# Kernel optimization log

Measured on AMD Instinct MI355X. Metric: run time of the kernel, lower is better.

## Reference

```python
import jax, jax.numpy as jnp
import numpy as np

B, T, C = 2, 2048, 1024
NH, NKV, HD = 16, 4, 64   # n_head, n_kv_head, head_dim
WIN_LEFT = 1024           # flash-attn window_size=(1024, 0), causal


def rmsnorm(x):
    # F.rms_norm with no weight: x / sqrt(mean(x^2) + eps), eps = dtype eps
    eps = jnp.finfo(x.dtype).eps
    return x * jax.lax.rsqrt(jnp.mean(x * x, axis=-1, keepdims=True) + eps)


def rope(x, cos, sin):
    # x: [B,T,H,D]; cos/sin: [T,1,D/2] broadcast over batch and heads
    d = x.shape[-1] // 2
    x1, x2 = x[..., :d], x[..., d:]
    return jnp.concatenate([x1 * cos + x2 * sin, -x1 * sin + x2 * cos], axis=-1)


def setup_inputs() -> dict:
    key = jax.random.key(0)
    ks = jax.random.split(key, 9)
    return {
        "x":  jax.random.normal(ks[0], (B, T, C), jnp.float32),
        "x0": jax.random.normal(ks[1], (B, T, C), jnp.float32),
        "ve": jax.random.normal(ks[2], (B, T, NKV, HD), jnp.float32),
        "cos": jax.random.normal(ks[3], (T, 1, HD // 2), jnp.float32),
        "sin": jax.random.normal(ks[4], (T, 1, HD // 2), jnp.float32),
        "Wq": jax.random.normal(ks[5], (NH * HD, C), jnp.float32) * 0.02,
        "Wk": jax.random.normal(ks[6], (NKV * HD, C), jnp.float32) * 0.02,
        "Wv": jax.random.normal(ks[7], (NKV * HD, C), jnp.float32) * 0.02,
        "Wo": jax.random.normal(ks[8], (C, C), jnp.float32) * 0.02,
    }


def reference(x, x0, ve, cos, sin, Wq, Wk, Wv, Wo):
    b, t, c = x.shape
    q = (x @ Wq.T).reshape(b, t, NH, HD)
    k = (x @ Wk.T).reshape(b, t, NKV, HD)
    v = (x @ Wv.T).reshape(b, t, NKV, HD)
    v_init = v
    # is_late branch: halve_value, add_init_qkv, add_init_v all active
    v = 0.5 * v
    x0n = rmsnorm(x0)
    q = 0.5 * q + 0.5 * (x0n @ Wq.T).reshape(b, t, NH, HD)
    k = 0.5 * k + 0.5 * (x0n @ Wk.T).reshape(b, t, NKV, HD)
    v = v + 0.5 * (x0n @ Wv.T).reshape(b, t, NKV, HD)
    v = v + 0.5 * ve
    # rotary -> rms-norm -> scale 1.2 on q and k
    q = rmsnorm(rope(q, cos, sin)) * 1.2
    k = rmsnorm(rope(k, cos, sin)) * 1.2
    # GQA: repeat kv heads to match query heads
    g = NH // NKV
    k = jnp.repeat(k, g, axis=2)
    v = jnp.repeat(v, g, axis=2)
    scores = jnp.einsum("bqhd,bkhd->bhqk", q, k) / np.float32(np.sqrt(HD))
    i = jnp.arange(t)[:, None]
    j = jnp.arange(t)[None, :]
    mask = (j <= i) & (i - j <= WIN_LEFT)  # causal sliding window
    scores = jnp.where(mask, scores, jnp.finfo(scores.dtype).min)
    att = jax.nn.softmax(scores, axis=-1)
    y = jnp.einsum("bhqk,bkhd->bqhd", att, v).reshape(b, t, c)
    y = y @ Wo.T
    return (y, v_init)
```

## Files before the change

kernel.cpp:

```cpp
#include <hip/hip_runtime.h>


typedef __attribute__((ext_vector_type(8))) short bf16x8;
typedef __attribute__((ext_vector_type(4))) float f32x4;
typedef unsigned short u16;
typedef unsigned int u32;

#define B_ 2
#define T_ 2048
#define C_ 1024
#define NH_ 16
#define NKV_ 4
#define HD_ 64
#define WIN_ 1024
#define M_ (B_*T_)
#define EPS_ 1.1920929e-07f

__device__ __forceinline__ u16 f2bf(float f) {
  u32 u = __float_as_uint(f);
  u32 r = (u + 0x7fffu + ((u >> 16) & 1u)) >> 16;
  return (u16)r;
}
__device__ __forceinline__ float bf2f(u16 h) { return __uint_as_float(((u32)h) << 16); }

__global__ __launch_bounds__(256) void k_convert(const float* __restrict__ src,
                                                 u16* __restrict__ dst, int n4) {
  int i = blockIdx.x * 256 + threadIdx.x;
  if (i >= n4) return;
  float4 v = ((const float4*)src)[i];
  ushort4 o;
  o.x = f2bf(v.x); o.y = f2bf(v.y); o.z = f2bf(v.z); o.w = f2bf(v.w);
  ((ushort4*)dst)[i] = o;
}

__global__ __launch_bounds__(256) void k_rms_combine(const float* __restrict__ x,
                                                     const float* __restrict__ x0,
                                                     u16* __restrict__ xbf,
                                                     u16* __restrict__ xmbf) {
  int row = blockIdx.x;
  int tid = threadIdx.x, lane = tid & 63, w = tid >> 6;
  const float4* px0 = (const float4*)(x0 + (size_t)row * C_);
  const float4* px  = (const float4*)(x  + (size_t)row * C_);
  float4 v0 = px0[tid];
  float ss = v0.x * v0.x + v0.y * v0.y + v0.z * v0.z + v0.w * v0.w;
  #pragma unroll
  for (int m = 1; m < 64; m <<= 1) ss += __shfl_xor(ss, m, 64);
  __shared__ float red[4];
  if (lane == 0) red[w] = ss;
  __syncthreads();
  float tot = red[0] + red[1] + red[2] + red[3];
  float rn = rsqrtf(tot * (1.0f / C_) + EPS_);
  float4 vx = px[tid];
  ushort4 om, ox;
  om.x = f2bf(0.5f * (vx.x + v0.x * rn));
  om.y = f2bf(0.5f * (vx.y + v0.y * rn));
  om.z = f2bf(0.5f * (vx.z + v0.z * rn));
  om.w = f2bf(0.5f * (vx.w + v0.w * rn));
  ox.x = f2bf(vx.x); ox.y = f2bf(vx.y); ox.z = f2bf(vx.z); ox.w = f2bf(vx.w);
  ((ushort4*)(xmbf + (size_t)row * C_))[tid] = om;
  ((ushort4*)(xbf  + (size_t)row * C_))[tid] = ox;
}

__device__ __forceinline__ void gemm_core(const u16* __restrict__ pa,
                                          const u16* __restrict__ pw,
                                          u16 (*As)[40], u16 (*Ws)[40],
                                          int lane, int r0, int c0,
                                          int ra, int ka, int rw, int kw,
                                          f32x4 acc[4][2]) {
  for (int kt = 0; kt < 1024; kt += 32) {
    int4 a0 = *(const int4*)(pa + kt);
    int4 a1 = *(const int4*)(pa + kt + 8);
    int4 w0 = *(const int4*)(pw + kt);
    __syncthreads();
    *(int4*)&As[ra][ka]     = a0;
    *(int4*)&As[ra][ka + 8] = a1;
    *(int4*)&Ws[rw][kw]     = w0;
    __syncthreads();
    bf16x8 af[4], bfr[2];
    #pragma unroll
    for (int fi = 0; fi < 4; fi++)
      af[fi] = *(const bf16x8*)&As[r0 + fi * 16 + (lane & 15)][(lane >> 4) * 8];
    #pragma unroll
    for (int fj = 0; fj < 2; fj++)
      bfr[fj] = *(const bf16x8*)&Ws[c0 + fj * 16 + (lane & 15)][(lane >> 4) * 8];
    #pragma unroll
    for (int fi = 0; fi < 4; fi++)
      #pragma unroll
      for (int fj = 0; fj < 2; fj++)
        acc[fi][fj] = __builtin_amdgcn_mfma_f32_16x16x32_bf16(af[fi], bfr[fj], acc[fi][fj], 0, 0, 0);
  }
}

__global__ __launch_bounds__(256) void k_gemm_qkv(const u16* __restrict__ xm,
                                                  const u16* __restrict__ xb,
                                                  const u16* __restrict__ Wq,
                                                  const u16* __restrict__ Wk,
                                                  const u16* __restrict__ Wv,
                                                  u16* __restrict__ qpre,
                                                  u16* __restrict__ kpre,
                                                  u16* __restrict__ vmid,
                                                  float* __restrict__ vinit) {
  __shared__ u16 As[128][40];
  __shared__ u16 Ws[64][40];
  int tid = threadIdx.x, lane = tid & 63, w = tid >> 6;
  int m0 = blockIdx.x * 128, bn = blockIdx.y, n0 = bn * 64;
  const u16* A; const u16* Wseg; int nseg;
  if (bn < 16)      { A = xm; Wseg = Wq; nseg = n0; }
  else if (bn < 20) { A = xm; Wseg = Wk; nseg = n0 - 1024; }
  else if (bn < 24) { A = xm; Wseg = Wv; nseg = n0 - 1280; }
  else              { A = xb; Wseg = Wv; nseg = n0 - 1536; }
  int ra = tid >> 1, ka = (tid & 1) * 16;
  int rw = tid >> 2, kw = (tid & 3) * 8;
  const u16* pa = A + (size_t)(m0 + ra) * 1024 + ka;
  const u16* pw = Wseg + (size_t)(nseg + rw) * 1024 + kw;
  int r0 = (w >> 1) * 64, c0 = (w & 1) * 32;
  f32x4 acc[4][2] = {};
  gemm_core(pa, pw, As, Ws, lane, r0, c0, ra, ka, rw, kw, acc);
  #pragma unroll
  for (int fi = 0; fi < 4; fi++)
    #pragma unroll
    for (int fj = 0; fj < 2; fj++)
      #pragma unroll
      for (int i = 0; i < 4; i++) {
        int m = m0 + r0 + fi * 16 + (lane >> 4) * 4 + i;
        int nl = nseg + c0 + fj * 16 + (lane & 15);
        float v = acc[fi][fj][i];
        if (bn < 16)      qpre[(size_t)m * 1024 + nl] = f2bf(v);
        else if (bn < 20) kpre[(size_t)m * 256 + nl] = f2bf(v);
        else if (bn < 24) vmid[(size_t)m * 256 + nl] = f2bf(v);
        else              vinit[(size_t)m * 256 + nl] = v;
      }
}

__global__ __launch_bounds__(256) void k_gemm_o(const u16* __restrict__ A,
                                                const u16* __restrict__ W,
                                                float* __restrict__ y) {
  __shared__ u16 As[128][40];
  __shared__ u16 Ws[64][40];
  int tid = threadIdx.x, lane = tid & 63, w = tid >> 6;
  int m0 = blockIdx.x * 128, n0 = blockIdx.y * 64;
  int ra = tid >> 1, ka = (tid & 1) * 16;
  int rw = tid >> 2, kw = (tid & 3) * 8;
  const u16* pa = A + (size_t)(m0 + ra) * 1024 + ka;
  const u16* pw = W + (size_t)(n0 + rw) * 1024 + kw;
  int r0 = (w >> 1) * 64, c0 = (w & 1) * 32;
  f32x4 acc[4][2] = {};
  gemm_core(pa, pw, As, Ws, lane, r0, c0, ra, ka, rw, kw, acc);
  #pragma unroll
  for (int fi = 0; fi < 4; fi++)
    #pragma unroll
    for (int fj = 0; fj < 2; fj++)
      #pragma unroll
      for (int i = 0; i < 4; i++) {
        int m = m0 + r0 + fi * 16 + (lane >> 4) * 4 + i;
        int n = n0 + c0 + fj * 16 + (lane & 15);
        y[(size_t)m * 1024 + n] = acc[fi][fj][i];
      }
}

__global__ __launch_bounds__(256) void k_qkv_post(const u16* __restrict__ qpre,
                                                  const u16* __restrict__ kpre,
                                                  const u16* __restrict__ vmid,
                                                  const float* __restrict__ ve,
                                                  const float* __restrict__ cosp,
                                                  const float* __restrict__ sinp,
                                                  u16* __restrict__ Qh,
                                                  u16* __restrict__ Kh,
                                                  u16* __restrict__ Vh) {
  int w = threadIdx.x >> 6, lane = threadIdx.x & 63;
  int vid = blockIdx.x * 4 + w;
  const int NQ = B_ * T_ * NH_;
  const int NK = B_ * T_ * NKV_;
  if (vid < NQ + NK) {
    int t, dstoff;
    float val;
    if (vid < NQ) {
      int h = vid & 15; t = (vid >> 4) & 2047; int b = vid >> 15;
      val = bf2f(qpre[(size_t)vid * 64 + lane]);
      dstoff = 0;
      size_t dst = (((size_t)(b * NH_ + h) * T_) + t) * 64 + lane;
      int di = lane & 31;
      float partner = __shfl_xor(val, 32, 64);
      float c = cosp[t * 32 + di], s = sinp[t * 32 + di];
      float r = (lane < 32) ? (val * c + partner * s) : (val * c - partner * s);
      float ss = r * r;
      #pragma unroll
      for (int m2 = 1; m2 < 64; m2 <<= 1) ss += __shfl_xor(ss, m2, 64);
      r *= rsqrtf(ss * (1.0f / 64.0f) + EPS_) * 1.2f;
      Qh[dst] = f2bf(r);
      (void)dstoff;
      return;
    } else {
      int kid = vid - NQ;
      int hk = kid & 3; t = (kid >> 2) & 2047; int b = kid >> 13;
      val = bf2f(kpre[(size_t)kid * 64 + lane]);
      size_t dst = (((size_t)(b * NKV_ + hk) * T_) + t) * 64 + lane;
      int di = lane & 31;
      float partner = __shfl_xor(val, 32, 64);
      float c = cosp[t * 32 + di], s = sinp[t * 32 + di];
      float r = (lane < 32) ? (val * c + partner * s) : (val * c - partner * s);
      float ss = r * r;
      #pragma unroll
      for (int m2 = 1; m2 < 64; m2 <<= 1) ss += __shfl_xor(ss, m2, 64);
      r *= rsqrtf(ss * (1.0f / 64.0f) + EPS_) * 1.2f;
      Kh[dst] = f2bf(r);
      return;
    }
  } else {
    int vvid = vid - NQ - NK;
    int hk = vvid & 3; int t = (vvid >> 2) & 2047; int b = vvid >> 13;
    float v = bf2f(vmid[(size_t)vvid * 64 + lane]) + 0.5f * ve[(size_t)vvid * 64 + lane];
    Vh[(((size_t)(b * NKV_ + hk) * T_) + t) * 64 + lane] = f2bf(v);
  }
}

__global__ __launch_bounds__(256) void k_attn(const u16* __restrict__ Qh,
                                              const u16* __restrict__ Kh,
                                              const u16* __restrict__ Vh,
                                              u16* __restrict__ ao) {
  __shared__ u16 Ks[64][72];
  __shared__ u16 Vt[64][72];
  __shared__ u16 Ps[4][16][72];
  int tid = threadIdx.x, lane = tid & 63, w = tid >> 6;
  int qt = blockIdx.x, h = blockIdx.y, b = blockIdx.z;
  int hk = h >> 2;
  const u16* Qp = Qh + ((size_t)(b * NH_ + h) * T_) * 64;
  const u16* Kp = Kh + ((size_t)(b * NKV_ + hk) * T_) * 64;
  const u16* Vp = Vh + ((size_t)(b * NKV_ + hk) * T_) * 64;
  int q0 = qt * 64;
  int qr = q0 + w * 16 + (lane & 15);
  bf16x8 qf[2];
  qf[0] = *(const bf16x8*)(Qp + (size_t)qr * 64 + (lane >> 4) * 8);
  qf[1] = *(const bf16x8*)(Qp + (size_t)qr * 64 + 32 + (lane >> 4) * 8);
  f32x4 o[4] = {};
  float mrun[4], lrun[4];
  #pragma unroll
  for (int i = 0; i < 4; i++) { mrun[i] = -1e4f; lrun[i] = 0.f; }
  int kt_lo = q0 - WIN_; if (kt_lo < 0) kt_lo = 0;
  int rk = tid >> 2, dk = (tid & 3) * 16;
  int kp2 = tid >> 3, dv = (tid & 7) * 8;
  for (int kt = kt_lo; kt <= q0; kt += 64) {
    int4 kv0 = *(const int4*)(Kp + (size_t)(kt + rk) * 64 + dk);
    int4 kv1 = *(const int4*)(Kp + (size_t)(kt + rk) * 64 + dk + 8);
    int4 va  = *(const int4*)(Vp + (size_t)(kt + 2 * kp2) * 64 + dv);
    int4 vb  = *(const int4*)(Vp + (size_t)(kt + 2 * kp2 + 1) * 64 + dv);
    __syncthreads();
    *(int4*)&Ks[rk][dk]     = kv0;
    *(int4*)&Ks[rk][dk + 8] = kv1;
    {
      const u16* sa = (const u16*)&va;
      const u16* sb = (const u16*)&vb;
      #pragma unroll
      for (int j = 0; j < 8; j++) {
        u32 valp = (u32)sa[j] | ((u32)sb[j] << 16);
        *(u32*)&Vt[dv + j][2 * kp2] = valp;
      }
    }
    __syncthreads();
    f32x4 s[4];
    #pragma unroll
    for (int ct = 0; ct < 4; ct++) {
      f32x4 z = {0.f, 0.f, 0.f, 0.f};
      s[ct] = z;
      #pragma unroll
      for (int kk = 0; kk < 2; kk++) {
        bf16x8 kf = *(const bf16x8*)&Ks[ct * 16 + (lane & 15)][kk * 32 + (lane >> 4) * 8];
        s[ct] = __builtin_amdgcn_mfma_f32_16x16x32_bf16(qf[kk], kf, s[ct], 0, 0, 0);
      }
    }
    int irow_base = q0 + w * 16 + (lane >> 4) * 4;
    float tmax[4];
    #pragma unroll
    for (int i = 0; i < 4; i++) tmax[i] = -1e30f;
    #pragma unroll
    for (int ct = 0; ct < 4; ct++) {
      int j = kt + ct * 16 + (lane & 15);
      #pragma unroll
      for (int i = 0; i < 4; i++) {
        int irow = irow_base + i;
        bool valid = (j <= irow) && (irow - j <= WIN_);
        float sv = valid ? s[ct][i] * 0.125f : -1e9f;
        s[ct][i] = sv;
        tmax[i] = fmaxf(tmax[i], sv);
      }
    }
    #pragma unroll
    for (int i = 0; i < 4; i++) {
      #pragma unroll
      for (int m2 = 1; m2 < 16; m2 <<= 1) tmax[i] = fmaxf(tmax[i], __shfl_xor(tmax[i], m2, 64));
    }
    float alpha[4];
    #pragma unroll
    for (int i = 0; i < 4; i++) {
      float mn = fmaxf(mrun[i], tmax[i]);
      alpha[i] = __expf(mrun[i] - mn);
      mrun[i] = mn;
    }
    float rsum[4] = {0.f, 0.f, 0.f, 0.f};
    #pragma unroll
    for (int ct = 0; ct < 4; ct++)
      #pragma unroll
      for (int i = 0; i < 4; i++) {
        float p = __expf(s[ct][i] - mrun[i]);
        s[ct][i] = p;
        rsum[i] += p;
      }
    #pragma unroll
    for (int i = 0; i < 4; i++) {
      #pragma unroll
      for (int m2 = 1; m2 < 16; m2 <<= 1) rsum[i] += __shfl_xor(rsum[i], m2, 64);
      lrun[i] = lrun[i] * alpha[i] + rsum[i];
    }
    #pragma unroll
    for (int fj = 0; fj < 4; fj++)
      #pragma unroll
      for (int i = 0; i < 4; i++) o[fj][i] *= alpha[i];
    #pragma unroll
    for (int ct = 0; ct < 4; ct++)
      #pragma unroll
      for (int i = 0; i < 4; i++)
        Ps[w][(lane >> 4) * 4 + i][ct * 16 + (lane & 15)] = f2bf(s[ct][i]);
    bf16x8 pf[2];
    pf[0] = *(const bf16x8*)&Ps[w][lane & 15][(lane >> 4) * 8];
    pf[1] = *(const bf16x8*)&Ps[w][lane & 15][32 + (lane >> 4) * 8];
    #pragma unroll
    for (int fj = 0; fj < 4; fj++) {
      #pragma unroll
      for (int ks = 0; ks < 2; ks++) {
        bf16x8 vf = *(const bf16x8*)&Vt[fj * 16 + (lane & 15)][ks * 32 + (lane >> 4) * 8];
        o[fj] = __builtin_amdgcn_mfma_f32_16x16x32_bf16(pf[ks], vf, o[fj], 0, 0, 0);
      }
    }
  }
  #pragma unroll
  for (int i = 0; i < 4; i++) {
    float inv = 1.0f / lrun[i];
    int irow = q0 + w * 16 + (lane >> 4) * 4 + i;
    size_t base = ((size_t)(b * T_ + irow) * NH_ + h) * 64;
    #pragma unroll
    for (int fj = 0; fj < 4; fj++)
      ao[base + fj * 16 + (lane & 15)] = f2bf(o[fj][i] * inv);
  }
}

extern "C" void kernel_launch(void* const* d_in, const int* in_sizes, int n_in,
                              void* d_out, int out_size, void* d_ws, size_t ws_size,
                              hipStream_t stream) {
  const float* x    = (const float*)d_in[0];
  const float* x0   = (const float*)d_in[1];
  const float* ve   = (const float*)d_in[2];
  const float* cosp = (const float*)d_in[3];
  const float* sinp = (const float*)d_in[4];
  const float* Wq   = (const float*)d_in[5];
  const float* Wk   = (const float*)d_in[6];
  const float* Wv   = (const float*)d_in[7];
  const float* Wo   = (const float*)d_in[8];
  float* out = (float*)d_out;

  u16* ws = (u16*)d_ws;
  size_t off = 0;
  u16* xbf  = ws + off; off += (size_t)M_ * C_;
  u16* xmbf = ws + off; off += (size_t)M_ * C_;
  u16* Wqb  = ws + off; off += (size_t)1024 * 1024;
  u16* Wkb  = ws + off; off += (size_t)256 * 1024;
  u16* Wvb  = ws + off; off += (size_t)256 * 1024;
  u16* Wob  = ws + off; off += (size_t)1024 * 1024;
  u16* qpre = ws + off; off += (size_t)M_ * 1024;
  u16* kpre = ws + off; off += (size_t)M_ * 256;
  u16* vmid = ws + off; off += (size_t)M_ * 256;
  u16* Vhb  = ws + off; off += (size_t)B_ * NKV_ * T_ * 64;
  u16* aob = xbf;
  u16* Qhb = xmbf;
  u16* Khb = Wqb;

  k_convert<<<1024, 256, 0, stream>>>(Wq, Wqb, 1024 * 1024 / 4);
  k_convert<<<256,  256, 0, stream>>>(Wk, Wkb, 256 * 1024 / 4);
  k_convert<<<256,  256, 0, stream>>>(Wv, Wvb, 256 * 1024 / 4);
  k_convert<<<1024, 256, 0, stream>>>(Wo, Wob, 1024 * 1024 / 4);
  k_rms_combine<<<4096, 256, 0, stream>>>(x, x0, xbf, xmbf);
  k_gemm_qkv<<<dim3(32, 28), 256, 0, stream>>>(xmbf, xbf, Wqb, Wkb, Wvb,
                                               qpre, kpre, vmid, out + (size_t)M_ * C_);
  k_qkv_post<<<24576, 256, 0, stream>>>(qpre, kpre, vmid, ve, cosp, sinp, Qhb, Khb, Vhb);
  k_attn<<<dim3(T_ / 64, NH_, B_), 256, 0, stream>>>(Qhb, Khb, Vhb, aob);
  k_gemm_o<<<dim3(32, 16), 256, 0, stream>>>(aob, Wob, out);
}
```

Before: 250.6 us.

## Use direct global-to-LDS loads with swizzle, pre-transpose V, merge converts

GEMM and attention tiles are now loaded with global_load_lds straight into XOR-swizzled LDS buffers, and the GEMM K-step grows from 32 to 64. The in-kernel V transpose is replaced by a separate kernel that writes V already transposed. Attention now skips the mask arithmetic on interior tiles and launches longest query tiles first. The four weight conversions become one launch, and Q/K post-processing is split from V handling. These changes target register staging, LDS bank conflicts and launch overhead, at the cost of an extra kernel and more code complexity.

After: 218.7 us. 12.7% less time.

```diff
diff --git a/kernel.cpp b/kernel.cpp
--- a/kernel.cpp
+++ b/kernel.cpp
@@ -11,7 +11,6 @@
 #define C_ 1024
 #define NH_ 16
 #define NKV_ 4
-#define HD_ 64
 #define WIN_ 1024
 #define M_ (B_*T_)
 #define EPS_ 1.1920929e-07f
@@ -23,14 +22,28 @@
 }
 __device__ __forceinline__ float bf2f(u16 h) { return __uint_as_float(((u32)h) << 16); }
 
-__global__ __launch_bounds__(256) void k_convert(const float* __restrict__ src,
-                                                 u16* __restrict__ dst, int n4) {
-  int i = blockIdx.x * 256 + threadIdx.x;
-  if (i >= n4) return;
-  float4 v = ((const float4*)src)[i];
+__device__ __forceinline__ void gload16(const u16* g, u16* l) {
+  __builtin_amdgcn_global_load_lds((const __attribute__((address_space(1))) u32*)g,
+                                   (__attribute__((address_space(3))) u32*)l, 16, 0, 0);
+}
+#define SWZ(row, kg) ((((row)) << 7) + ((((kg) ^ ((row) & 7))) << 4))
+#define SWO(lane) (8 * (((lane) & 7) ^ (((lane) >> 3) & 7)))
+
+__global__ __launch_bounds__(256) void k_convert_all(const float* __restrict__ Wq,
+                                                     const float* __restrict__ Wk,
+                                                     const float* __restrict__ Wv,
+                                                     const float* __restrict__ Wo,
+                                                     u16* __restrict__ dst) {
+  int i4 = blockIdx.x * 256 + threadIdx.x;
+  const float* src; int s0;
+  if (i4 < 262144)      { src = Wq; s0 = 0; }
+  else if (i4 < 327680) { src = Wk; s0 = 262144; }
+  else if (i4 < 393216) { src = Wv; s0 = 327680; }
+  else                  { src = Wo; s0 = 393216; }
+  float4 v = ((const float4*)src)[i4 - s0];
   ushort4 o;
   o.x = f2bf(v.x); o.y = f2bf(v.y); o.z = f2bf(v.z); o.w = f2bf(v.w);
-  ((ushort4*)dst)[i] = o;
+  ((ushort4*)dst)[i4] = o;
 }
 
 __global__ __launch_bounds__(256) void k_rms_combine(const float* __restrict__ x,
@@ -61,33 +74,38 @@
   ((ushort4*)(xbf  + (size_t)row * C_))[tid] = ox;
 }
 
-__device__ __forceinline__ void gemm_core(const u16* __restrict__ pa,
-                                          const u16* __restrict__ pw,
-                                          u16 (*As)[40], u16 (*Ws)[40],
-                                          int lane, int r0, int c0,
-                                          int ra, int ka, int rw, int kw,
+__device__ __forceinline__ void gemm_core(const u16* pa0, const u16* pb0,
+                                          u16* Asl, u16* Bsl,
+                                          int lane, int w, int r0, int c0,
                                           f32x4 acc[4][2]) {
-  for (int kt = 0; kt < 1024; kt += 32) {
-    int4 a0 = *(const int4*)(pa + kt);
-    int4 a1 = *(const int4*)(pa + kt + 8);
-    int4 w0 = *(const int4*)(pw + kt);
+  const char* Ab = (const char*)Asl;
+  const char* Bb = (const char*)Bsl;
+  for (int kt = 0; kt < 1024; kt += 64) {
     __syncthreads();
-    *(int4*)&As[ra][ka]     = a0;
-    *(int4*)&As[ra][ka + 8] = a1;
-    *(int4*)&Ws[rw][kw]     = w0;
+    #pragma unroll
+    for (int c = 0; c < 4; c++)
+      gload16(pa0 + (size_t)c * 32 * 1024 + kt, Asl + (c * 32 + w * 8) * 64);
+    #pragma unroll
+    for (int c = 0; c < 2; c++)
+      gload16(pb0 + (size_t)c * 32 * 1024 + kt, Bsl + (c * 32 + w * 8) * 64);
     __syncthreads();
-    bf16x8 af[4], bfr[2];
-    #pragma unroll
-    for (int fi = 0; fi < 4; fi++)
-      af[fi] = *(const bf16x8*)&As[r0 + fi * 16 + (lane & 15)][(lane >> 4) * 8];
-    #pragma unroll
-    for (int fj = 0; fj < 2; fj++)
-      bfr[fj] = *(const bf16x8*)&Ws[c0 + fj * 16 + (lane & 15)][(lane >> 4) * 8];
-    #pragma unroll
-    for (int fi = 0; fi < 4; fi++)
+    bf16x8 af[2][4], bfr[2][2];
+    #pragma unroll
+    for (int ks = 0; ks < 2; ks++) {
+      #pragma unroll
+      for (int fi = 0; fi < 4; fi++)
+        af[ks][fi] = *(const bf16x8*)(Ab + SWZ(r0 + fi * 16 + (lane & 15), ks * 4 + (lane >> 4)));
       #pragma unroll
       for (int fj = 0; fj < 2; fj++)
-        acc[fi][fj] = __builtin_amdgcn_mfma_f32_16x16x32_bf16(af[fi], bfr[fj], acc[fi][fj], 0, 0, 0);
+        bfr[ks][fj] = *(const bf16x8*)(Bb + SWZ(c0 + fj * 16 + (lane & 15), ks * 4 + (lane >> 4)));
+    }
+    #pragma unroll
+    for (int ks = 0; ks < 2; ks++)
+      #pragma unroll
+      for (int fi = 0; fi < 4; fi++)
+        #pragma unroll
+        for (int fj = 0; fj < 2; fj++)
+          acc[fi][fj] = __builtin_amdgcn_mfma_f32_16x16x32_bf16(af[ks][fi], bfr[ks][fj], acc[fi][fj], 0, 0, 0);
   }
 }
 
@@ -100,8 +118,8 @@
                                                   u16* __restrict__ kpre,
                                                   u16* __restrict__ vmid,
                                                   float* __restrict__ vinit) {
-  __shared__ u16 As[128][40];
-  __shared__ u16 Ws[64][40];
+  __shared__ u16 Asl[128 * 64];
+  __shared__ u16 Bsl[64 * 64];
   int tid = threadIdx.x, lane = tid & 63, w = tid >> 6;
   int m0 = blockIdx.x * 128, bn = blockIdx.y, n0 = bn * 64;
   const u16* A; const u16* Wseg; int nseg;
@@ -109,13 +127,12 @@
   else if (bn < 20) { A = xm; Wseg = Wk; nseg = n0 - 1024; }
   else if (bn < 24) { A = xm; Wseg = Wv; nseg = n0 - 1280; }
   else              { A = xb; Wseg = Wv; nseg = n0 - 1536; }
-  int ra = tid >> 1, ka = (tid & 1) * 16;
-  int rw = tid >> 2, kw = (tid & 3) * 8;
-  const u16* pa = A + (size_t)(m0 + ra) * 1024 + ka;
-  const u16* pw = Wseg + (size_t)(nseg + rw) * 1024 + kw;
+  int swo = SWO(lane);
+  const u16* pa0 = A    + (size_t)(m0 + w * 8 + (lane >> 3)) * 1024 + swo;
+  const u16* pb0 = Wseg + (size_t)(nseg + w * 8 + (lane >> 3)) * 1024 + swo;
   int r0 = (w >> 1) * 64, c0 = (w & 1) * 32;
   f32x4 acc[4][2] = {};
-  gemm_core(pa, pw, As, Ws, lane, r0, c0, ra, ka, rw, kw, acc);
+  gemm_core(pa0, pb0, Asl, Bsl, lane, w, r0, c0, acc);
   #pragma unroll
   for (int fi = 0; fi < 4; fi++)
     #pragma unroll
@@ -135,17 +152,16 @@
 __global__ __launch_bounds__(256) void k_gemm_o(const u16* __restrict__ A,
                                                 const u16* __restrict__ W,
                                                 float* __restrict__ y) {
-  __shared__ u16 As[128][40];
-  __shared__ u16 Ws[64][40];
+  __shared__ u16 Asl[128 * 64];
+  __shared__ u16 Bsl[64 * 64];
   int tid = threadIdx.x, lane = tid & 63, w = tid >> 6;
   int m0 = blockIdx.x * 128, n0 = blockIdx.y * 64;
-  int ra = tid >> 1, ka = (tid & 1) * 16;
-  int rw = tid >> 2, kw = (tid & 3) * 8;
-  const u16* pa = A + (size_t)(m0 + ra) * 1024 + ka;
-  const u16* pw = W + (size_t)(n0 + rw) * 1024 + kw;
+  int swo = SWO(lane);
+  const u16* pa0 = A + (size_t)(m0 + w * 8 + (lane >> 3)) * 1024 + swo;
+  const u16* pb0 = W + (size_t)(n0 + w * 8 + (lane >> 3)) * 1024 + swo;
   int r0 = (w >> 1) * 64, c0 = (w & 1) * 32;
   f32x4 acc[4][2] = {};
-  gemm_core(pa, pw, As, Ws, lane, r0, c0, ra, ka, rw, kw, acc);
+  gemm_core(pa0, pb0, Asl, Bsl, lane, w, r0, c0, acc);
   #pragma unroll
   for (int fi = 0; fi < 4; fi++)
     #pragma unroll
@@ -158,103 +174,108 @@
       }
 }
 
-__global__ __launch_bounds__(256) void k_qkv_post(const u16* __restrict__ qpre,
-                                                  const u16* __restrict__ kpre,
-                                                  const u16* __restrict__ vmid,
-                                                  const float* __restrict__ ve,
-                                                  const float* __restrict__ cosp,
-                                                  const float* __restrict__ sinp,
-                                                  u16* __restrict__ Qh,
-                                                  u16* __restrict__ Kh,
-                                                  u16* __restrict__ Vh) {
+__global__ __launch_bounds__(256) void k_qk_post(const u16* __restrict__ qpre,
+                                                 const u16* __restrict__ kpre,
+                                                 const float* __restrict__ cosp,
+                                                 const float* __restrict__ sinp,
+                                                 u16* __restrict__ Qh,
+                                                 u16* __restrict__ Kh) {
   int w = threadIdx.x >> 6, lane = threadIdx.x & 63;
   int vid = blockIdx.x * 4 + w;
   const int NQ = B_ * T_ * NH_;
-  const int NK = B_ * T_ * NKV_;
-  if (vid < NQ + NK) {
-    int t, dstoff;
-    float val;
-    if (vid < NQ) {
-      int h = vid & 15; t = (vid >> 4) & 2047; int b = vid >> 15;
-      val = bf2f(qpre[(size_t)vid * 64 + lane]);
-      dstoff = 0;
-      size_t dst = (((size_t)(b * NH_ + h) * T_) + t) * 64 + lane;
-      int di = lane & 31;
-      float partner = __shfl_xor(val, 32, 64);
-      float c = cosp[t * 32 + di], s = sinp[t * 32 + di];
-      float r = (lane < 32) ? (val * c + partner * s) : (val * c - partner * s);
-      float ss = r * r;
-      #pragma unroll
-      for (int m2 = 1; m2 < 64; m2 <<= 1) ss += __shfl_xor(ss, m2, 64);
-      r *= rsqrtf(ss * (1.0f / 64.0f) + EPS_) * 1.2f;
-      Qh[dst] = f2bf(r);
-      (void)dstoff;
-      return;
-    } else {
-      int kid = vid - NQ;
-      int hk = kid & 3; t = (kid >> 2) & 2047; int b = kid >> 13;
-      val = bf2f(kpre[(size_t)kid * 64 + lane]);
-      size_t dst = (((size_t)(b * NKV_ + hk) * T_) + t) * 64 + lane;
-      int di = lane & 31;
-      float partner = __shfl_xor(val, 32, 64);
-      float c = cosp[t * 32 + di], s = sinp[t * 32 + di];
-      float r = (lane < 32) ? (val * c + partner * s) : (val * c - partner * s);
-      float ss = r * r;
-      #pragma unroll
-      for (int m2 = 1; m2 < 64; m2 <<= 1) ss += __shfl_xor(ss, m2, 64);
-      r *= rsqrtf(ss * (1.0f / 64.0f) + EPS_) * 1.2f;
-      Kh[dst] = f2bf(r);
-      return;
-    }
+  int t; float val; size_t dst; u16* out;
+  if (vid < NQ) {
+    int h = vid & 15; t = (vid >> 4) & 2047; int b = vid >> 15;
+    val = bf2f(qpre[(size_t)vid * 64 + lane]);
+    dst = (((size_t)(b * NH_ + h) * T_) + t) * 64 + lane;
+    out = Qh;
   } else {
-    int vvid = vid - NQ - NK;
-    int hk = vvid & 3; int t = (vvid >> 2) & 2047; int b = vvid >> 13;
-    float v = bf2f(vmid[(size_t)vvid * 64 + lane]) + 0.5f * ve[(size_t)vvid * 64 + lane];
-    Vh[(((size_t)(b * NKV_ + hk) * T_) + t) * 64 + lane] = f2bf(v);
+    int kid = vid - NQ;
+    int hk = kid & 3; t = (kid >> 2) & 2047; int b = kid >> 13;
+    val = bf2f(kpre[(size_t)kid * 64 + lane]);
+    dst = (((size_t)(b * NKV_ + hk) * T_) + t) * 64 + lane;
+    out = Kh;
+  }
+  int di = lane & 31;
+  float partner = __shfl_xor(val, 32, 64);
+  float c = cosp[t * 32 + di], s = sinp[t * 32 + di];
+  float r = (lane < 32) ? (val * c + partner * s) : (val * c - partner * s);
+  float ss = r * r;
+  #pragma unroll
+  for (int m2 = 1; m2 < 64; m2 <<= 1) ss += __shfl_xor(ss, m2, 64);
+  r *= rsqrtf(ss * (1.0f / 64.0f) + EPS_) * 1.2f;
+  out[dst] = f2bf(r);
+}
+
+__global__ __launch_bounds__(256) void k_vt(const u16* __restrict__ vmid,
+                                            const float* __restrict__ ve,
+                                            u16* __restrict__ VtG) {
+  __shared__ u16 S[64][72];
+  int tid = threadIdx.x;
+  int t0 = blockIdx.x * 64, hk = blockIdx.y, b = blockIdx.z;
+  {
+    int tl = tid >> 2, dg = (tid & 3) * 16;
+    const int4* pvm = (const int4*)(vmid + (size_t)(b * T_ + t0 + tl) * 256 + hk * 64 + dg);
+    const float4* pve = (const float4*)(ve + ((size_t)(b * T_ + t0 + tl) * 4 + hk) * 64 + dg);
+    int4 vv[2]; vv[0] = pvm[0]; vv[1] = pvm[1];
+    const u16* vm = (const u16*)vv;
+    float4 vf[4]; vf[0] = pve[0]; vf[1] = pve[1]; vf[2] = pve[2]; vf[3] = pve[3];
+    const float* vfp = (const float*)vf;
+    u16 r[16];
+    #pragma unroll
+    for (int e = 0; e < 16; e++) r[e] = f2bf(bf2f(vm[e]) + 0.5f * vfp[e]);
+    *(int4*)&S[tl][dg] = *(int4*)&r[0];
+    *(int4*)&S[tl][dg + 8] = *(int4*)&r[8];
+  }
+  __syncthreads();
+  {
+    int dl = tid >> 2, tg = (tid & 3) * 16;
+    u16 r[16];
+    #pragma unroll
+    for (int j = 0; j < 16; j++) r[j] = S[tg + j][dl];
+    u16* o = VtG + ((size_t)((b * NKV_ + hk) * 64 + dl)) * T_ + t0 + tg;
+    *(int4*)&o[0] = *(int4*)&r[0];
+    *(int4*)&o[8] = *(int4*)&r[8];
   }
 }
 
 __global__ __launch_bounds__(256) void k_attn(const u16* __restrict__ Qh,
                                               const u16* __restrict__ Kh,
-                                              const u16* __restrict__ Vh,
+                                              const u16* __restrict__ VtG,
                                               u16* __restrict__ ao) {
-  __shared__ u16 Ks[64][72];
-  __shared__ u16 Vt[64][72];
+  __shared__ u16 Ksl[64 * 64];
+  __shared__ u16 Vsl[64 * 64];
   __shared__ u16 Ps[4][16][72];
   int tid = threadIdx.x, lane = tid & 63, w = tid >> 6;
-  int qt = blockIdx.x, h = blockIdx.y, b = blockIdx.z;
+  int qt = (int)gridDim.x - 1 - (int)blockIdx.x;
+  int h = blockIdx.y, b = blockIdx.z;
   int hk = h >> 2;
+  int q0 = qt * 64;
   const u16* Qp = Qh + ((size_t)(b * NH_ + h) * T_) * 64;
   const u16* Kp = Kh + ((size_t)(b * NKV_ + hk) * T_) * 64;
-  const u16* Vp = Vh + ((size_t)(b * NKV_ + hk) * T_) * 64;
-  int q0 = qt * 64;
+  int swo = SWO(lane);
+  const u16* pk0 = Kp + (size_t)(w * 8 + (lane >> 3)) * 64 + swo;
+  const u16* pv0 = VtG + ((size_t)((b * NKV_ + hk) * 64 + w * 8 + (lane >> 3))) * T_ + swo;
+  const char* Kb = (const char*)Ksl;
+  const char* Vb = (const char*)Vsl;
+
   int qr = q0 + w * 16 + (lane & 15);
   bf16x8 qf[2];
   qf[0] = *(const bf16x8*)(Qp + (size_t)qr * 64 + (lane >> 4) * 8);
   qf[1] = *(const bf16x8*)(Qp + (size_t)qr * 64 + 32 + (lane >> 4) * 8);
+
   f32x4 o[4] = {};
   float mrun[4], lrun[4];
   #pragma unroll
   for (int i = 0; i < 4; i++) { mrun[i] = -1e4f; lrun[i] = 0.f; }
   int kt_lo = q0 - WIN_; if (kt_lo < 0) kt_lo = 0;
-  int rk = tid >> 2, dk = (tid & 3) * 16;
-  int kp2 = tid >> 3, dv = (tid & 7) * 8;
+
   for (int kt = kt_lo; kt <= q0; kt += 64) {
-    int4 kv0 = *(const int4*)(Kp + (size_t)(kt + rk) * 64 + dk);
-    int4 kv1 = *(const int4*)(Kp + (size_t)(kt + rk) * 64 + dk + 8);
-    int4 va  = *(const int4*)(Vp + (size_t)(kt + 2 * kp2) * 64 + dv);
-    int4 vb  = *(const int4*)(Vp + (size_t)(kt + 2 * kp2 + 1) * 64 + dv);
     __syncthreads();
-    *(int4*)&Ks[rk][dk]     = kv0;
-    *(int4*)&Ks[rk][dk + 8] = kv1;
-    {
-      const u16* sa = (const u16*)&va;
-      const u16* sb = (const u16*)&vb;
-      #pragma unroll
-      for (int j = 0; j < 8; j++) {
-        u32 valp = (u32)sa[j] | ((u32)sb[j] << 16);
-        *(u32*)&Vt[dv + j][2 * kp2] = valp;
-      }
+    #pragma unroll
+    for (int c = 0; c < 2; c++) {
+      gload16(pk0 + (size_t)(kt + c * 32) * 64, Ksl + (c * 32 + w * 8) * 64);
+      gload16(pv0 + kt + (size_t)c * 32 * T_,   Vsl + (c * 32 + w * 8) * 64);
     }
     __syncthreads();
     f32x4 s[4];
@@ -263,26 +284,36 @@
       f32x4 z = {0.f, 0.f, 0.f, 0.f};
       s[ct] = z;
       #pragma unroll
-      for (int kk = 0; kk < 2; kk++) {
-        bf16x8 kf = *(const bf16x8*)&Ks[ct * 16 + (lane & 15)][kk * 32 + (lane >> 4) * 8];
-        s[ct] = __builtin_amdgcn_mfma_f32_16x16x32_bf16(qf[kk], kf, s[ct], 0, 0, 0);
-      }
-    }
-    int irow_base = q0 + w * 16 + (lane >> 4) * 4;
-    float tmax[4];
-    #pragma unroll
-    for (int i = 0; i < 4; i++) tmax[i] = -1e30f;
-    #pragma unroll
-    for (int ct = 0; ct < 4; ct++) {
-      int j = kt + ct * 16 + (lane & 15);
-      #pragma unroll
-      for (int i = 0; i < 4; i++) {
-        int irow = irow_base + i;
-        bool valid = (j <= irow) && (irow - j <= WIN_);
-        float sv = valid ? s[ct][i] * 0.125f : -1e9f;
-        s[ct][i] = sv;
-        tmax[i] = fmaxf(tmax[i], sv);
-      }
+      for (int ks = 0; ks < 2; ks++) {
+        bf16x8 kf = *(const bf16x8*)(Kb + SWZ(ct * 16 + (lane & 15), ks * 4 + (lane >> 4)));
+        s[ct] = __builtin_amdgcn_mfma_f32_16x16x32_bf16(qf[ks], kf, s[ct], 0, 0, 0);
+      }
+    }
+    bool need_mask = (kt == q0) || (kt == q0 - WIN_);
+    int irow0 = q0 + w * 16 + (lane >> 4) * 4;
+    float tmax[4] = {-1e30f, -1e30f, -1e30f, -1e30f};
+    if (need_mask) {
+      #pragma unroll
+      for (int ct = 0; ct < 4; ct++) {
+        int j = kt + ct * 16 + (lane & 15);
+        #pragma unroll
+        for (int i = 0; i < 4; i++) {
+          int irow = irow0 + i;
+          bool valid = (j <= irow) && (irow - j <= WIN_);
+          float sv = valid ? s[ct][i] * 0.125f : -1e9f;
+          s[ct][i] = sv;
+          tmax[i] = fmaxf(tmax[i], sv);
+        }
+      }
+    } else {
+      #pragma unroll
+      for (int ct = 0; ct < 4; ct++)
+        #pragma unroll
+        for (int i = 0; i < 4; i++) {
+          float sv = s[ct][i] * 0.125f;
+          s[ct][i] = sv;
+          tmax[i] = fmaxf(tmax[i], sv);
+        }
     }
     #pragma unroll
     for (int i = 0; i < 4; i++) {
@@ -327,7 +358,7 @@
     for (int fj = 0; fj < 4; fj++) {
       #pragma unroll
       for (int ks = 0; ks < 2; ks++) {
-        bf16x8 vf = *(const bf16x8*)&Vt[fj * 16 + (lane & 15)][ks * 32 + (lane >> 4) * 8];
+        bf16x8 vf = *(const bf16x8*)(Vb + SWZ(fj * 16 + (lane & 15), ks * 4 + (lane >> 4)));
         o[fj] = __builtin_amdgcn_mfma_f32_16x16x32_bf16(pf[ks], vf, o[fj], 0, 0, 0);
       }
     }
@@ -368,19 +399,17 @@
   u16* qpre = ws + off; off += (size_t)M_ * 1024;
   u16* kpre = ws + off; off += (size_t)M_ * 256;
   u16* vmid = ws + off; off += (size_t)M_ * 256;
-  u16* Vhb  = ws + off; off += (size_t)B_ * NKV_ * T_ * 64;
+  u16* VtG  = ws + off; off += (size_t)B_ * NKV_ * 64 * T_;
   u16* aob = xbf;
   u16* Qhb = xmbf;
   u16* Khb = Wqb;
 
-  k_convert<<<1024, 256, 0, stream>>>(Wq, Wqb, 1024 * 1024 / 4);
-  k_convert<<<256,  256, 0, stream>>>(Wk, Wkb, 256 * 1024 / 4);
-  k_convert<<<256,  256, 0, stream>>>(Wv, Wvb, 256 * 1024 / 4);
-  k_convert<<<1024, 256, 0, stream>>>(Wo, Wob, 1024 * 1024 / 4);
+  k_convert_all<<<2560, 256, 0, stream>>>(Wq, Wk, Wv, Wo, Wqb);
   k_rms_combine<<<4096, 256, 0, stream>>>(x, x0, xbf, xmbf);
   k_gemm_qkv<<<dim3(32, 28), 256, 0, stream>>>(xmbf, xbf, Wqb, Wkb, Wvb,
                                                qpre, kpre, vmid, out + (size_t)M_ * C_);
-  k_qkv_post<<<24576, 256, 0, stream>>>(qpre, kpre, vmid, ve, cosp, sinp, Qhb, Khb, Vhb);
-  k_attn<<<dim3(T_ / 64, NH_, B_), 256, 0, stream>>>(Qhb, Khb, Vhb, aob);
+  k_qk_post<<<20480, 256, 0, stream>>>(qpre, kpre, cosp, sinp, Qhb, Khb);
+  k_vt<<<dim3(32, 4, 2), 256, 0, stream>>>(vmid, ve, VtG);
+  k_attn<<<dim3(32, 16, 2), 256, 0, stream>>>(Qhb, Khb, VtG, aob);
   k_gemm_o<<<dim3(32, 16), 256, 0, stream>>>(aob, Wob, out);
 }
```
